# Optimization experiments

Measured on AMD Instinct MI355X. Metric: run time of the kernel, lower is better.

Reference implementation:

```python
import jax, jax.numpy as jnp
import numpy as np

B, T, F = 64, 1024, 4
INF = jnp.float32(1e30)


def _dtw_cost(p, q):
    """Accumulated DTW cost matrix. p: [T1,2], q: [T2,2]. Returns C: [T1,T2].

    Recurrence C[i,j] = D[i,j] + min(C[i-1,j], C[i,j-1], C[i-1,j-1]).
    The within-row dependency c_j = d_j + min(a_j, c_{j-1}) (with
    a_j = min(C[i-1,j], C[i-1,j-1])) is a min-plus scan, solved in closed
    form: c_j = S_j + cummin_k<=j (a_k - S_{k-1}), S = cumsum(d).
    """
    # pairwise Euclidean distance (dtw.dtw2d uses 2D Euclidean)
    D = jnp.sqrt(jnp.sum((p[:, None, :] - q[None, :, :]) ** 2, axis=-1))  # [T1,T2]

    c0 = jnp.cumsum(D[0])  # first row: only left moves allowed

    def row(prev, d):
        shifted = jnp.concatenate([jnp.full((1,), INF, prev.dtype), prev[:-1]])
        a = jnp.minimum(prev, shifted)          # min(C[i-1,j], C[i-1,j-1])
        S = jnp.cumsum(d)
        Sprev = jnp.concatenate([jnp.zeros((1,), d.dtype), S[:-1]])
        m = jax.lax.associative_scan(jnp.minimum, a - Sprev)
        c = S + m
        return c, c

    _, rest = jax.lax.scan(row, c0, D[1:])
    return jnp.concatenate([c0[None, :], rest], axis=0)


def _dtw_path(C):
    """Backtrace alignment path from C. Returns (a, b, valid) each [T1+T2-1]."""
    T1, T2 = C.shape
    L = T1 + T2 - 1

    def step(carry, _):
        i, j, done = carry
        at0 = (i == 0) & (j == 0)
        cd = jnp.where((i > 0) & (j > 0), C[i - 1, j - 1], INF)
        cu = jnp.where(i > 0, C[i - 1, j], INF)
        cl = jnp.where(j > 0, C[i, j - 1], INF)
        k = jnp.argmin(jnp.stack([cd, cu, cl]))  # diag preferred on ties
        di = jnp.where(k == 2, 0, 1)
        dj = jnp.where(k == 1, 0, 1)
        ni = jnp.where(at0, 0, i - di)
        nj = jnp.where(at0, 0, j - dj)
        return (ni, nj, done | at0), (i, j, jnp.logical_not(done))

    init = (jnp.int32(T1 - 1), jnp.int32(T2 - 1), jnp.bool_(False))
    _, (a, b, valid) = jax.lax.scan(step, init, None, length=L)
    return a, b, valid


def _single_loss(pred, targ, subcoef):
    # DTW alignment computed on (x, y) basis, detached (torch runs it in numpy)
    p = jax.lax.stop_gradient(pred[:, :2])
    q = jax.lax.stop_gradient(targ[:, :2])
    C = _dtw_cost(p, q)
    a, b, valid = _dtw_path(C)
    # gather aligned points on loss_indices = [0, 1], L1 loss weighted by subcoef
    pg = pred[a, :2]  # [L, 2]
    tg = targ[b, :2]
    w = valid[:, None].astype(pred.dtype)
    return jnp.sum(jnp.abs(pg - tg) * subcoef[None, :] * w)


def setup_inputs() -> dict:
    key = jax.random.key(0)
    k1, k2 = jax.random.split(key)
    preds = jax.random.normal(k1, (B, T, F), dtype=jnp.float32)
    targs = jax.random.normal(k2, (B, T, F), dtype=jnp.float32)
    subcoef = jnp.ones((2,), dtype=jnp.float32)
    return {"preds": preds, "targs": targs, "subcoef": subcoef}


def reference(preds, targs, subcoef):
    losses = jax.vmap(lambda p, t: _single_loss(p, t, subcoef))(preds, targs)
    return jnp.sum(losses)
```

## Files before the change

### kernel.cpp

```cpp
#include <hip/hip_runtime.h>

#define TT   1024
#define NW   34
#define NPH  (NW + 21)
#define FINF 1e30f

template<bool A> struct BoolC { static constexpr bool value = A; };


__device__ __forceinline__ float dpp_shr1_old(float oldv, float x) {
    return __int_as_float(__builtin_amdgcn_update_dpp(
        __float_as_int(oldv), __float_as_int(x), 0x138, 0xF, 0xF, false));
}

__global__ __launch_bounds__(512) void dtw_forward(
    const float* __restrict__ preds,
    const float* __restrict__ targs,
    uint2* __restrict__ dirs)
{
    __shared__ float2 qsh[TT];
    __shared__ float  mbox[7][TT];

    if (blockIdx.x & 3) return;
    const int b = blockIdx.x >> 2;

    const int tid  = threadIdx.x;
    const int w    = tid >> 6;
    const int lane = tid & 63;

    for (int k = tid; k < TT; k += 512) {
        float4 t4 = ((const float4*)targs)[(size_t)b * TT + k];
        qsh[k] = make_float2(t4.x, t4.y);
    }
    for (int k = tid; k < 7 * TT; k += 512) ((float*)mbox)[k] = FINF;

    float px0, py0, px1, py1;
    {
        const int row0 = w * 128 + 2 * lane;
        float4 pv = ((const float4*)preds)[(size_t)b * TT + row0];
        px0 = pv.x; py0 = pv.y;
        float4 pw = ((const float4*)preds)[(size_t)b * TT + row0 + 1];
        px1 = pw.x; py1 = pw.y;
    }
    __syncthreads();

    const float* src = (w > 0) ? mbox[w - 1] : nullptr;
    float*       dst = (w < 7) ? mbox[w]     : nullptr;

    float cur0 = FINF, cur1 = FINF, uprev = FINF, ucur = FINF;
    unsigned au0 = 0, ad0 = 0, au1 = 0, ad1 = 0;
    unsigned pau0 = 0, pad0 = 0, pau1 = 0, pad1 = 0;
    int pT = -1;

    const int bi  = 2 * w + (lane >> 5);
    const int rr0 = 2 * (lane & 31);
    const bool is63 = (lane == 63);

    for (int G = 0; G < NPH; ++G) {
        if (pT >= 0) {
            const size_t base = (size_t)((b * 16 + bi) * NW + pT) * 64 + rr0;
            *(uint4*)&dirs[base] =
                make_uint4(__builtin_bitreverse32(pau0), __builtin_bitreverse32(pad0),
                           __builtin_bitreverse32(pau1), __builtin_bitreverse32(pad1));
            pT = -1;
        }
        const int T = G - 3 * w;
        if ((unsigned)T < (unsigned)NW) {
            float bnd[33];
#pragma unroll
            for (int k = 0; k < 33; ++k) bnd[k] = FINF;
            if (w > 0) {
#pragma unroll
                for (int k = 0; k < 33; ++k) {
                    const int c = 32 * T + k;
                    if (c < TT) bnd[k] = src[c];
                }
            }
            if (T == 0) ucur = bnd[0];
            float qx[32], qy[32];
#pragma unroll
            for (int k = 0; k < 32; ++k) {
                float2 v = qsh[(32 * T + k - lane) & (TT - 1)];
                qx[k] = v.x; qy[k] = v.y;
            }
            float bq[32];
            auto body = [&](auto actc) {
                constexpr bool ACT = decltype(actc)::value;
#pragma unroll
                for (int k2 = 0; k2 < 32; ++k2) {
                    const int s = 32 * T + k2;
                    const float dx0 = px0 - qx[k2], dy0 = py0 - qy[k2];
                    const float d0 = __builtin_amdgcn_sqrtf(dx0 * dx0 + dy0 * dy0);
                    const float dx1 = px1 - qx[k2], dy1 = py1 - qy[k2];
                    const float d1 = __builtin_amdgcn_sqrtf(dx1 * dx1 + dy1 * dy1);

                    const float u = ucur;
                    float ba0 = fminf(fminf(u, cur0), uprev);
                    const unsigned bd0 = (uprev == ba0) ? 1u : 0u;
                    const unsigned bu0 = ((u <= cur0) ? 1u : 0u) | bd0;
                    if constexpr (ACT) ba0 = (ba0 > 9e29f) ? 0.0f : ba0;
                    const float v0 = d0 + ba0;
                    const float ba1 = fminf(fminf(v0, cur1), cur0);
                    const unsigned bd1 = (cur0 == ba1) ? 1u : 0u;
                    const unsigned bu1 = ((v0 <= cur1) ? 1u : 0u) | bd1;
                    const float v1 = d1 + ba1;

                    au0 = au0 + au0 + bu0;  ad0 = ad0 + ad0 + bd0;
                    au1 = au1 + au1 + bu1;  ad1 = ad1 + ad1 + bd1;

                    if constexpr (ACT) {
                        const bool act = (lane <= s);
                        cur0 = act ? v0 : cur0;
                        cur1 = act ? v1 : cur1;
                    } else {
                        cur0 = v0; cur1 = v1;
                    }
                    uprev = u;
                    bq[k2] = cur1;
                    ucur = dpp_shr1_old(bnd[k2 + 1], cur1);
                }
            };
            if (T < 2) body(BoolC<true>{}); else body(BoolC<false>{});

            if (is63 && w < 7) {
#pragma unroll
                for (int k2 = 0; k2 < 32; ++k2) {
                    const int c = 32 * T + k2 - 63;
                    if ((unsigned)c < 1024u) dst[c] = bq[k2];
                }
            }
            pau0 = au0; pad0 = ad0; pau1 = au1; pad1 = ad1; pT = T;
            au0 = ad0 = au1 = ad1 = 0u;
        }
        __syncthreads();
    }
    if (pT >= 0) {
        const size_t base = (size_t)((b * 16 + bi) * NW + pT) * 64 + rr0;
        *(uint4*)&dirs[base] =
            make_uint4(__builtin_bitreverse32(pau0), __builtin_bitreverse32(pad0),
                       __builtin_bitreverse32(pau1), __builtin_bitreverse32(pad1));
    }
}

__global__ __launch_bounds__(1024) void dtw_exits(
    const uint2* __restrict__ dirs,
    unsigned short* __restrict__ exitc)
{
    __shared__ uint2 raw[NW * 64];
    __shared__ unsigned nebit[64][32];
    __shared__ unsigned dgbit[64][32];

    const int tid = threadIdx.x;
    const int b = blockIdx.x >> 4, bi = blockIdx.x & 15;

    for (int i = tid; i < NW * 64; i += 1024)
        raw[i] = dirs[(size_t)(b * 16 + bi) * (NW * 64) + i];
    __syncthreads();
    for (int i = tid; i < 64 * 32; i += 1024) {
        const int rr = i >> 5, u = i & 31;
        const int o  = ((bi & 1) << 5) + (rr >> 1);
        const int T0 = u + (o >> 5), sh = o & 31;
        uint2 A  = raw[T0 * 64 + rr];
        uint2 Bv = raw[(T0 + 1) * 64 + rr];
        nebit[rr][u] = sh ? ((A.x >> sh) | (Bv.x << (32 - sh))) : A.x;
        dgbit[rr][u] = sh ? ((A.y >> sh) | (Bv.y << (32 - sh))) : A.y;
    }
    __syncthreads();

    int j = tid;
    for (int rr = 63; rr >= 0; --rr) {
        if (bi == 0 && rr == 0) { j = 0; break; }
        int u = j >> 5, m = j & 31;
        unsigned wv = nebit[rr][u] << (31 - m);
        while (wv == 0u && u > 0) { --u; wv = nebit[rr][u]; m = 31; }
        const int j2 = (wv == 0u) ? 0 : ((u << 5) + m - __builtin_clz(wv));
        const int diag = (int)((dgbit[rr][j2 >> 5] >> (j2 & 31)) & 1u);
        j = j2 - diag;
        if (j < 0) j = 0;
    }
    exitc[((size_t)(b * 16 + bi) << 10) + tid] = (unsigned short)j;
}

__global__ __launch_bounds__(64) void dtw_loss(
    const float* __restrict__ preds,
    const float* __restrict__ targs,
    const float* __restrict__ subcoef,
    const uint2* __restrict__ dirs,
    const unsigned short* __restrict__ exitc,
    float* __restrict__ out)
{
    __shared__ uint2 raw[NW * 64];
    __shared__ unsigned nebit[64][32];
    __shared__ unsigned dgbit[64][32];
    __shared__ float2 qsh[TT];
    __shared__ float2 psh[64];
    __shared__ unsigned recs[160];

    const int lane = threadIdx.x;
    const int b = blockIdx.x >> 4, bi = blockIdx.x & 15;

    for (int i = lane; i < NW * 64; i += 64)
        raw[i] = dirs[(size_t)(b * 16 + bi) * (NW * 64) + i];
    for (int k = lane; k < TT; k += 64) {
        float4 t4 = ((const float4*)targs)[(size_t)b * TT + k];
        qsh[k] = make_float2(t4.x, t4.y);
    }
    {
        float4 p4 = ((const float4*)preds)[(size_t)b * TT + bi * 64 + lane];
        psh[lane] = make_float2(p4.x, p4.y);
    }
    __syncthreads();
    for (int i = lane; i < 64 * 32; i += 64) {
        const int rr = i >> 5, u = i & 31;
        const int o  = ((bi & 1) << 5) + (rr >> 1);
        const int T0 = u + (o >> 5), sh = o & 31;
        uint2 A  = raw[T0 * 64 + rr];
        uint2 Bv = raw[(T0 + 1) * 64 + rr];
        nebit[rr][u] = sh ? ((A.x >> sh) | (Bv.x << (32 - sh))) : A.x;
        dgbit[rr][u] = sh ? ((A.y >> sh) | (Bv.y << (32 - sh))) : A.y;
    }

    int j = TT - 1;
    for (int k = 15; k > bi; --k)
        j = exitc[((size_t)(b * 16 + k) << 10) + j];
    __syncthreads();

    int nrec = 0;
    for (int rr = 63; rr >= 0; --rr) {
        int j2;
        if (bi == 0 && rr == 0) j2 = 0;
        else {
            int u = j >> 5, m = j & 31;
            unsigned wv = nebit[rr][u] << (31 - m);
            while (wv == 0u && u > 0) { --u; wv = nebit[rr][u]; m = 31; }
            j2 = (wv == 0u) ? 0 : ((u << 5) + m - __builtin_clz(wv));
        }
        int c = j;
        for (;;) {
            int cl = (c - 31 > j2) ? (c - 31) : j2;
            if (lane == 0)
                recs[nrec] = ((unsigned)rr << 20) | ((unsigned)cl << 10) | (unsigned)c;
            ++nrec;
            if (cl == j2) break;
            c = cl - 1;
        }
        if (bi == 0 && rr == 0) j = 0;
        else {
            const int diag = (int)((dgbit[rr][j2 >> 5] >> (j2 & 31)) & 1u);
            j = j2 - diag;
            if (j < 0) j = 0;
        }
    }
    __syncthreads();

    const float sc0 = subcoef[0], sc1 = subcoef[1];
    float acc = 0.0f;
    for (int k = lane; k < nrec; k += 64) {
        unsigned rec = recs[k];
        int rr = (int)(rec >> 20), cl = (int)((rec >> 10) & 1023u), ch = (int)(rec & 1023u);
        float2 p = psh[rr];
        for (int c = cl; c <= ch; ++c) {
            float2 q = qsh[c];
            acc += fabsf(p.x - q.x) * sc0 + fabsf(p.y - q.y) * sc1;
        }
    }
    for (int o = 32; o; o >>= 1) acc += __shfl_down(acc, o);
    if (lane == 0) atomicAdd(out, acc);
}

extern "C" void kernel_launch(void* const* d_in, const int* in_sizes, int n_in,
                              void* d_out, int out_size, void* d_ws, size_t ws_size,
                              hipStream_t stream)
{
    const float* preds   = (const float*)d_in[0];
    const float* targs   = (const float*)d_in[1];
    const float* subcoef = (const float*)d_in[2];
    float* out = (float*)d_out;

    const int B = in_sizes[0] / (TT * 4);

    const size_t dirsBytes = (size_t)B * 16 * NW * 64 * sizeof(uint2);
    uint2* dirs = (uint2*)d_ws;
    unsigned short* exitc = (unsigned short*)((char*)d_ws + dirsBytes);

    hipMemsetAsync(out, 0, sizeof(float), stream);
    dtw_forward<<<dim3(B * 4), dim3(512), 0, stream>>>(preds, targs, dirs);
    dtw_exits<<<dim3(B * 16), dim3(1024), 0, stream>>>(dirs, exitc);
    dtw_loss<<<dim3(B * 16), dim3(64), 0, stream>>>(preds, targs, subcoef, dirs, exitc, out);
}
```

Baseline: 409.7 us.

## Fuse DTW forward, exit computation and backtrace loss into one per-batch kernel

Merges the three kernels into one block per batch element. After the forward pass, the block walks the backtrace sequentially band by band, with double-buffered staging of the next band's direction bits by other warps. A precomputed per-word 'last nonzero' table replaces the backward word scan, and shared memory is XOR-swizzled. This removes the all-columns exit pass and two launches, and trims the idle blocks of the old forward grid. In exchange the backtrace becomes serial across 16 bands inside one block, and the loss accumulation loses the cross-block parallelism it had before.

```diff
diff --git a/kernel.cpp b/kernel.cpp
--- a/kernel.cpp
+++ b/kernel.cpp
@@ -13,26 +13,31 @@
         __float_as_int(oldv), __float_as_int(x), 0x138, 0xF, 0xF, false));
 }
 
-__global__ __launch_bounds__(512) void dtw_forward(
+#define POOL_BYTES 50852
+#define SWZ(rr, u) ((u) ^ ((rr) & 31))
+
+__global__ __launch_bounds__(512) void dtw_fused(
     const float* __restrict__ preds,
     const float* __restrict__ targs,
-    uint2* __restrict__ dirs)
+    const float* __restrict__ subcoef,
+    uint2* __restrict__ dirs,
+    float* __restrict__ out)
 {
     __shared__ float2 qsh[TT];
-    __shared__ float  mbox[7][TT];
-
-    if (blockIdx.x & 3) return;
-    const int b = blockIdx.x >> 2;
+    __shared__ __align__(16) char pool[POOL_BYTES];
+
+    float (*mbox)[TT] = (float (*)[TT])pool;
 
     const int tid  = threadIdx.x;
     const int w    = tid >> 6;
     const int lane = tid & 63;
+    const int b    = blockIdx.x;
 
     for (int k = tid; k < TT; k += 512) {
         float4 t4 = ((const float4*)targs)[(size_t)b * TT + k];
         qsh[k] = make_float2(t4.x, t4.y);
     }
-    for (int k = tid; k < 7 * TT; k += 512) ((float*)mbox)[k] = FINF;
+    for (int k = tid; k < 7 * TT; k += 512) ((float*)pool)[k] = FINF;
 
     float px0, py0, px1, py1;
     {
@@ -44,228 +49,219 @@
     }
     __syncthreads();
 
-    const float* src = (w > 0) ? mbox[w - 1] : nullptr;
-    float*       dst = (w < 7) ? mbox[w]     : nullptr;
-
-    float cur0 = FINF, cur1 = FINF, uprev = FINF, ucur = FINF;
-    unsigned au0 = 0, ad0 = 0, au1 = 0, ad1 = 0;
-    unsigned pau0 = 0, pad0 = 0, pau1 = 0, pad1 = 0;
-    int pT = -1;
-
-    const int bi  = 2 * w + (lane >> 5);
-    const int rr0 = 2 * (lane & 31);
-    const bool is63 = (lane == 63);
-
-    for (int G = 0; G < NPH; ++G) {
+    {
+        const float* src = (w > 0) ? mbox[w - 1] : nullptr;
+        float*       dst = (w < 7) ? mbox[w]     : nullptr;
+
+        float cur0 = FINF, cur1 = FINF, uprev = FINF, ucur = FINF;
+        unsigned au0 = 0, ad0 = 0, au1 = 0, ad1 = 0;
+        unsigned pau0 = 0, pad0 = 0, pau1 = 0, pad1 = 0;
+        int pT = -1;
+
+        const int bi  = 2 * w + (lane >> 5);
+        const int rr0 = 2 * (lane & 31);
+        const bool is63 = (lane == 63);
+
+        for (int G = 0; G < NPH; ++G) {
+            if (pT >= 0) {
+                const size_t base = (size_t)((b * 16 + bi) * NW + pT) * 64 + rr0;
+                *(uint4*)&dirs[base] =
+                    make_uint4(__builtin_bitreverse32(pau0), __builtin_bitreverse32(pad0),
+                               __builtin_bitreverse32(pau1), __builtin_bitreverse32(pad1));
+                pT = -1;
+            }
+            const int T = G - 3 * w;
+            if ((unsigned)T < (unsigned)NW) {
+                float bnd[33];
+#pragma unroll
+                for (int k = 0; k < 33; ++k) bnd[k] = FINF;
+                if (w > 0) {
+#pragma unroll
+                    for (int k = 0; k < 33; ++k) {
+                        const int c = 32 * T + k;
+                        if (c < TT) bnd[k] = src[c];
+                    }
+                }
+                if (T == 0) ucur = bnd[0];
+                float qx[32], qy[32];
+#pragma unroll
+                for (int k = 0; k < 32; ++k) {
+                    float2 v = qsh[(32 * T + k - lane) & (TT - 1)];
+                    qx[k] = v.x; qy[k] = v.y;
+                }
+                float bq[32];
+                auto body = [&](auto actc) {
+                    constexpr bool ACT = decltype(actc)::value;
+#pragma unroll
+                    for (int k2 = 0; k2 < 32; ++k2) {
+                        const int s = 32 * T + k2;
+                        const float dx0 = px0 - qx[k2], dy0 = py0 - qy[k2];
+                        const float d0 = __builtin_amdgcn_sqrtf(dx0 * dx0 + dy0 * dy0);
+                        const float dx1 = px1 - qx[k2], dy1 = py1 - qy[k2];
+                        const float d1 = __builtin_amdgcn_sqrtf(dx1 * dx1 + dy1 * dy1);
+
+                        const float u = ucur;
+                        float ba0 = fminf(fminf(u, cur0), uprev);
+                        const unsigned bd0 = (uprev == ba0) ? 1u : 0u;
+                        const unsigned bu0 = ((u <= cur0) ? 1u : 0u) | bd0;
+                        if constexpr (ACT) ba0 = (ba0 > 9e29f) ? 0.0f : ba0;
+                        const float v0 = d0 + ba0;
+                        const float ba1 = fminf(fminf(v0, cur1), cur0);
+                        const unsigned bd1 = (cur0 == ba1) ? 1u : 0u;
+                        const unsigned bu1 = ((v0 <= cur1) ? 1u : 0u) | bd1;
+                        const float v1 = d1 + ba1;
+
+                        au0 = au0 + au0 + bu0;  ad0 = ad0 + ad0 + bd0;
+                        au1 = au1 + au1 + bu1;  ad1 = ad1 + ad1 + bd1;
+
+                        if constexpr (ACT) {
+                            const bool act = (lane <= s);
+                            cur0 = act ? v0 : cur0;
+                            cur1 = act ? v1 : cur1;
+                        } else {
+                            cur0 = v0; cur1 = v1;
+                        }
+                        uprev = u;
+                        bq[k2] = cur1;
+                        ucur = dpp_shr1_old(bnd[k2 + 1], cur1);
+                    }
+                };
+                if (T < 2) body(BoolC<true>{}); else body(BoolC<false>{});
+
+                if (is63 && w < 7) {
+#pragma unroll
+                    for (int k2 = 0; k2 < 32; ++k2) {
+                        const int c = 32 * T + k2 - 63;
+                        if ((unsigned)c < 1024u) dst[c] = bq[k2];
+                    }
+                }
+                pau0 = au0; pad0 = ad0; pau1 = au1; pad1 = ad1; pT = T;
+                au0 = ad0 = au1 = ad1 = 0u;
+            }
+            __syncthreads();
+        }
         if (pT >= 0) {
             const size_t base = (size_t)((b * 16 + bi) * NW + pT) * 64 + rr0;
             *(uint4*)&dirs[base] =
                 make_uint4(__builtin_bitreverse32(pau0), __builtin_bitreverse32(pad0),
                            __builtin_bitreverse32(pau1), __builtin_bitreverse32(pad1));
-            pT = -1;
-        }
-        const int T = G - 3 * w;
-        if ((unsigned)T < (unsigned)NW) {
-            float bnd[33];
-#pragma unroll
-            for (int k = 0; k < 33; ++k) bnd[k] = FINF;
-            if (w > 0) {
-#pragma unroll
-                for (int k = 0; k < 33; ++k) {
-                    const int c = 32 * T + k;
-                    if (c < TT) bnd[k] = src[c];
-                }
-            }
-            if (T == 0) ucur = bnd[0];
-            float qx[32], qy[32];
-#pragma unroll
-            for (int k = 0; k < 32; ++k) {
-                float2 v = qsh[(32 * T + k - lane) & (TT - 1)];
-                qx[k] = v.x; qy[k] = v.y;
-            }
-            float bq[32];
-            auto body = [&](auto actc) {
-                constexpr bool ACT = decltype(actc)::value;
-#pragma unroll
-                for (int k2 = 0; k2 < 32; ++k2) {
-                    const int s = 32 * T + k2;
-                    const float dx0 = px0 - qx[k2], dy0 = py0 - qy[k2];
-                    const float d0 = __builtin_amdgcn_sqrtf(dx0 * dx0 + dy0 * dy0);
-                    const float dx1 = px1 - qx[k2], dy1 = py1 - qy[k2];
-                    const float d1 = __builtin_amdgcn_sqrtf(dx1 * dx1 + dy1 * dy1);
-
-                    const float u = ucur;
-                    float ba0 = fminf(fminf(u, cur0), uprev);
-                    const unsigned bd0 = (uprev == ba0) ? 1u : 0u;
-                    const unsigned bu0 = ((u <= cur0) ? 1u : 0u) | bd0;
-                    if constexpr (ACT) ba0 = (ba0 > 9e29f) ? 0.0f : ba0;
-                    const float v0 = d0 + ba0;
-                    const float ba1 = fminf(fminf(v0, cur1), cur0);
-                    const unsigned bd1 = (cur0 == ba1) ? 1u : 0u;
-                    const unsigned bu1 = ((v0 <= cur1) ? 1u : 0u) | bd1;
-                    const float v1 = d1 + ba1;
-
-                    au0 = au0 + au0 + bu0;  ad0 = ad0 + ad0 + bd0;
-                    au1 = au1 + au1 + bu1;  ad1 = ad1 + ad1 + bd1;
-
-                    if constexpr (ACT) {
-                        const bool act = (lane <= s);
-                        cur0 = act ? v0 : cur0;
-                        cur1 = act ? v1 : cur1;
-                    } else {
-                        cur0 = v0; cur1 = v1;
-                    }
-                    uprev = u;
-                    bq[k2] = cur1;
-                    ucur = dpp_shr1_old(bnd[k2 + 1], cur1);
-                }
-            };
-            if (T < 2) body(BoolC<true>{}); else body(BoolC<false>{});
-
-            if (is63 && w < 7) {
-#pragma unroll
-                for (int k2 = 0; k2 < 32; ++k2) {
-                    const int c = 32 * T + k2 - 63;
-                    if ((unsigned)c < 1024u) dst[c] = bq[k2];
-                }
-            }
-            pau0 = au0; pad0 = ad0; pau1 = au1; pad1 = ad1; pT = T;
-            au0 = ad0 = au1 = ad1 = 0u;
-        }
-        __syncthreads();
-    }
-    if (pT >= 0) {
-        const size_t base = (size_t)((b * 16 + bi) * NW + pT) * 64 + rr0;
-        *(uint4*)&dirs[base] =
-            make_uint4(__builtin_bitreverse32(pau0), __builtin_bitreverse32(pad0),
-                       __builtin_bitreverse32(pau1), __builtin_bitreverse32(pad1));
-    }
-}
-
-__global__ __launch_bounds__(1024) void dtw_exits(
-    const uint2* __restrict__ dirs,
-    unsigned short* __restrict__ exitc)
-{
-    __shared__ uint2 raw[NW * 64];
-    __shared__ unsigned nebit[64][32];
-    __shared__ unsigned dgbit[64][32];
-
-    const int tid = threadIdx.x;
-    const int b = blockIdx.x >> 4, bi = blockIdx.x & 15;
-
-    for (int i = tid; i < NW * 64; i += 1024)
-        raw[i] = dirs[(size_t)(b * 16 + bi) * (NW * 64) + i];
-    __syncthreads();
-    for (int i = tid; i < 64 * 32; i += 1024) {
-        const int rr = i >> 5, u = i & 31;
-        const int o  = ((bi & 1) << 5) + (rr >> 1);
-        const int T0 = u + (o >> 5), sh = o & 31;
-        uint2 A  = raw[T0 * 64 + rr];
-        uint2 Bv = raw[(T0 + 1) * 64 + rr];
-        nebit[rr][u] = sh ? ((A.x >> sh) | (Bv.x << (32 - sh))) : A.x;
-        dgbit[rr][u] = sh ? ((A.y >> sh) | (Bv.y << (32 - sh))) : A.y;
-    }
-    __syncthreads();
-
-    int j = tid;
-    for (int rr = 63; rr >= 0; --rr) {
-        if (bi == 0 && rr == 0) { j = 0; break; }
-        int u = j >> 5, m = j & 31;
-        unsigned wv = nebit[rr][u] << (31 - m);
-        while (wv == 0u && u > 0) { --u; wv = nebit[rr][u]; m = 31; }
-        const int j2 = (wv == 0u) ? 0 : ((u << 5) + m - __builtin_clz(wv));
-        const int diag = (int)((dgbit[rr][j2 >> 5] >> (j2 & 31)) & 1u);
-        j = j2 - diag;
-        if (j < 0) j = 0;
-    }
-    exitc[((size_t)(b * 16 + bi) << 10) + tid] = (unsigned short)j;
-}
-
-__global__ __launch_bounds__(64) void dtw_loss(
-    const float* __restrict__ preds,
-    const float* __restrict__ targs,
-    const float* __restrict__ subcoef,
-    const uint2* __restrict__ dirs,
-    const unsigned short* __restrict__ exitc,
-    float* __restrict__ out)
-{
-    __shared__ uint2 raw[NW * 64];
-    __shared__ unsigned nebit[64][32];
-    __shared__ unsigned dgbit[64][32];
-    __shared__ float2 qsh[TT];
-    __shared__ float2 psh[64];
-    __shared__ unsigned recs[160];
-
-    const int lane = threadIdx.x;
-    const int b = blockIdx.x >> 4, bi = blockIdx.x & 15;
-
-    for (int i = lane; i < NW * 64; i += 64)
-        raw[i] = dirs[(size_t)(b * 16 + bi) * (NW * 64) + i];
-    for (int k = lane; k < TT; k += 64) {
-        float4 t4 = ((const float4*)targs)[(size_t)b * TT + k];
-        qsh[k] = make_float2(t4.x, t4.y);
-    }
-    {
-        float4 p4 = ((const float4*)preds)[(size_t)b * TT + bi * 64 + lane];
-        psh[lane] = make_float2(p4.x, p4.y);
-    }
-    __syncthreads();
-    for (int i = lane; i < 64 * 32; i += 64) {
-        const int rr = i >> 5, u = i & 31;
-        const int o  = ((bi & 1) << 5) + (rr >> 1);
-        const int T0 = u + (o >> 5), sh = o & 31;
-        uint2 A  = raw[T0 * 64 + rr];
-        uint2 Bv = raw[(T0 + 1) * 64 + rr];
-        nebit[rr][u] = sh ? ((A.x >> sh) | (Bv.x << (32 - sh))) : A.x;
-        dgbit[rr][u] = sh ? ((A.y >> sh) | (Bv.y << (32 - sh))) : A.y;
-    }
-
-    int j = TT - 1;
-    for (int k = 15; k > bi; --k)
-        j = exitc[((size_t)(b * 16 + k) << 10) + j];
-    __syncthreads();
-
-    int nrec = 0;
-    for (int rr = 63; rr >= 0; --rr) {
-        int j2;
-        if (bi == 0 && rr == 0) j2 = 0;
-        else {
-            int u = j >> 5, m = j & 31;
-            unsigned wv = nebit[rr][u] << (31 - m);
-            while (wv == 0u && u > 0) { --u; wv = nebit[rr][u]; m = 31; }
-            j2 = (wv == 0u) ? 0 : ((u << 5) + m - __builtin_clz(wv));
-        }
-        int c = j;
-        for (;;) {
-            int cl = (c - 31 > j2) ? (c - 31) : j2;
-            if (lane == 0)
-                recs[nrec] = ((unsigned)rr << 20) | ((unsigned)cl << 10) | (unsigned)c;
-            ++nrec;
-            if (cl == j2) break;
-            c = cl - 1;
-        }
-        if (bi == 0 && rr == 0) j = 0;
-        else {
-            const int diag = (int)((dgbit[rr][j2 >> 5] >> (j2 & 31)) & 1u);
-            j = j2 - diag;
-            if (j < 0) j = 0;
-        }
-    }
+        }
+    }
+    __syncthreads();
+
+    unsigned (*ne)[64][32] = (unsigned (*)[64][32])(pool);
+    unsigned (*dg)[64][32] = (unsigned (*)[64][32])(pool + 16384);
+    unsigned (*zd)[64][32] = (unsigned (*)[64][32])(pool + 32768);
+    float2 (*psh)[64]      = (float2 (*)[64])(pool + 49152);
+    unsigned* recs         = (unsigned*)(pool + 50176);
+    unsigned* nrecp        = (unsigned*)(pool + 50816);
+    float* wsum            = (float*)(pool + 50820);
+
+    auto stage = [&](int band, int buf) {
+        if (tid >= 64 && tid < 128) {
+            const int rr = tid - 64;
+            const size_t gbase = (size_t)(b * 16 + band) * (NW * 64);
+            const int o  = ((band & 1) << 5) + (rr >> 1);
+            const int sh = o & 31;
+            const int Tb = o >> 5;
+            unsigned run = 0;
+#pragma unroll 4
+            for (int u = 0; u < 32; ++u) {
+                uint2 A  = dirs[gbase + (size_t)(u + Tb) * 64 + rr];
+                uint2 Bv = dirs[gbase + (size_t)(u + Tb + 1) * 64 + rr];
+                const unsigned nw = sh ? ((A.x >> sh) | (Bv.x << (32 - sh))) : A.x;
+                const unsigned dw = sh ? ((A.y >> sh) | (Bv.y << (32 - sh))) : A.y;
+                ne[buf][rr][SWZ(rr, u)] = nw;
+                dg[buf][rr][SWZ(rr, u)] = dw;
+                zd[buf][rr][SWZ(rr, u)] = run;
+                if (nw != 0u) {
+                    const int bit = 31 - __builtin_clz(nw);
+                    const int c = (u << 5) + bit;
+                    int jn = c - (int)((dw >> bit) & 1u);
+                    if (jn < 0) jn = 0;
+                    run = ((unsigned)c << 10) | (unsigned)jn;
+                }
+            }
+        } else if (tid >= 128 && tid < 192) {
+            const int rr = tid - 128;
+            float4 p4 = ((const float4*)preds)[(size_t)b * TT + band * 64 + rr];
+            psh[buf][rr] = make_float2(p4.x, p4.y);
+        }
+    };
+
+    stage(15, 0);
     __syncthreads();
 
     const float sc0 = subcoef[0], sc1 = subcoef[1];
     float acc = 0.0f;
-    for (int k = lane; k < nrec; k += 64) {
-        unsigned rec = recs[k];
-        int rr = (int)(rec >> 20), cl = (int)((rec >> 10) & 1023u), ch = (int)(rec & 1023u);
-        float2 p = psh[rr];
-        for (int c = cl; c <= ch; ++c) {
-            float2 q = qsh[c];
-            acc += fabsf(p.x - q.x) * sc0 + fabsf(p.y - q.y) * sc1;
-        }
-    }
+    int j = TT - 1;
+    int cur = 0;
+
+    for (int band = 15; band >= 0; --band) {
+        if (w == 0) {
+            int nrec = 0;
+#pragma unroll 1
+            for (int rr = 63; rr >= 0; --rr) {
+                int j2, jn;
+                if (band == 0 && rr == 0) { j2 = 0; jn = 0; }
+                else {
+                    const int u = j >> 5, m = j & 31;
+                    const unsigned nw = ne[cur][rr][SWZ(rr, u)];
+                    const unsigned dw = dg[cur][rr][SWZ(rr, u)];
+                    const unsigned z  = zd[cur][rr][SWZ(rr, u)];
+                    const unsigned wv = nw << (31 - m);
+                    if (wv != 0u) {
+                        j2 = (u << 5) + m - __builtin_clz(wv);
+                        jn = j2 - (int)((dw >> (j2 & 31)) & 1u);
+                        if (jn < 0) jn = 0;
+                    } else {
+                        j2 = (int)(z >> 10);
+                        jn = (int)(z & 1023u);
+                    }
+                }
+                int c = j;
+                for (;;) {
+                    const int cl = (c - 31 > j2) ? (c - 31) : j2;
+                    if (lane == 0)
+                        recs[nrec] = ((unsigned)rr << 20) | ((unsigned)cl << 10) | (unsigned)c;
+                    ++nrec;
+                    if (cl == j2) break;
+                    c = cl - 1;
+                }
+                j = jn;
+            }
+            if (lane == 0) *nrecp = (unsigned)nrec;
+        } else if (band > 0) {
+            stage(band - 1, cur ^ 1);
+        }
+        __syncthreads();
+
+        const int nr = (int)*nrecp;
+        const float2* pb = psh[cur];
+        for (int k = tid; k < nr; k += 512) {
+            const unsigned rec = recs[k];
+            const int rr = (int)(rec >> 20);
+            const int cl = (int)((rec >> 10) & 1023u);
+            const int ch = (int)(rec & 1023u);
+            const float2 p = pb[rr];
+            for (int c = cl; c <= ch; ++c) {
+                const float2 q = qsh[c];
+                acc += fabsf(p.x - q.x) * sc0 + fabsf(p.y - q.y) * sc1;
+            }
+        }
+        __syncthreads();
+        cur ^= 1;
+    }
+
     for (int o = 32; o; o >>= 1) acc += __shfl_down(acc, o);
-    if (lane == 0) atomicAdd(out, acc);
+    if (lane == 0) wsum[w] = acc;
+    __syncthreads();
+    if (tid == 0) {
+        float s = 0.0f;
+#pragma unroll
+        for (int k = 0; k < 8; ++k) s += wsum[k];
+        atomicAdd(out, s);
+    }
 }
 
 extern "C" void kernel_launch(void* const* d_in, const int* in_sizes, int n_in,
@@ -279,12 +275,8 @@
 
     const int B = in_sizes[0] / (TT * 4);
 
-    const size_t dirsBytes = (size_t)B * 16 * NW * 64 * sizeof(uint2);
     uint2* dirs = (uint2*)d_ws;
-    unsigned short* exitc = (unsigned short*)((char*)d_ws + dirsBytes);
 
     hipMemsetAsync(out, 0, sizeof(float), stream);
-    dtw_forward<<<dim3(B * 4), dim3(512), 0, stream>>>(preds, targs, dirs);
-    dtw_exits<<<dim3(B * 16), dim3(1024), 0, stream>>>(dirs, exitc);
-    dtw_loss<<<dim3(B * 16), dim3(64), 0, stream>>>(preds, targs, subcoef, dirs, exitc, out);
+    dtw_fused<<<dim3(B), dim3(512), 0, stream>>>(preds, targs, subcoef, dirs, out);
 }
```

Result: slower. 509.9 us (+24.5%).
